# Kernel tuning notes

Hardware: AMD Instinct MI355X
Metric: run time of the kernel (lower is better)

The kernel has to match this reference:

```python
import jax, jax.numpy as jnp
import numpy as np
import math

D_MODEL = 2048
R = 512
N_HEADS = 16
D_K = R // N_HEADS  # 32
B = 2
S = 2048


def _xavier(key, out_dim, in_dim):
    limit = math.sqrt(6.0 / (in_dim + out_dim))
    return jax.random.uniform(key, (out_dim, in_dim), jnp.float32, -limit, limit)


def setup_inputs() -> dict:
    key = jax.random.key(0)
    ks = jax.random.split(key, 6)
    x = jax.random.normal(ks[0], (B, S, D_MODEL), dtype=jnp.float32)
    mask = jnp.ones((B, 1, 1, S), dtype=jnp.int32)
    # torch nn.Linear weights have shape (out, in)
    Wq = _xavier(ks[1], R, D_MODEL)
    Wk = _xavier(ks[2], R, D_MODEL)
    Wv = _xavier(ks[3], R, D_MODEL)
    Wo = _xavier(ks[4], D_MODEL, R)
    bq = jnp.zeros((R,), jnp.float32)
    bk = jnp.zeros((R,), jnp.float32)
    bv = jnp.zeros((R,), jnp.float32)
    bo = jnp.zeros((D_MODEL,), jnp.float32)
    return {"x": x, "Wq": Wq, "bq": bq, "Wk": Wk, "bk": bk,
            "Wv": Wv, "bv": bv, "Wo": Wo, "bo": bo, "mask": mask}


def reference(x, Wq, bq, Wk, bk, Wv, bv, Wo, bo, mask):
    b, s, _ = x.shape
    scale = math.sqrt(D_K)
    # projections: (B,S,d_model) @ (d_model,r) -> (B,S,r)
    Q = x @ Wq.T + bq
    K = x @ Wk.T + bk
    V = x @ Wv.T + bv
    # (B,S,r) -> (B,H,S,d_k)
    Q = Q.reshape(b, s, N_HEADS, D_K).transpose(0, 2, 1, 3)
    K = K.reshape(b, s, N_HEADS, D_K).transpose(0, 2, 1, 3)
    V = V.reshape(b, s, N_HEADS, D_K).transpose(0, 2, 1, 3)
    # scores: (B,H,Sq,Sk)
    scores = jnp.einsum('bhqd,bhkd->bhqk', Q, K) / scale
    scores = jnp.where(mask == 0, -jnp.inf, scores)
    attn = jax.nn.softmax(scores, axis=-1)  # dropout p=0 (eval)
    out = jnp.einsum('bhqk,bhkd->bhqd', attn, V)
    out = out.transpose(0, 2, 1, 3).reshape(b, s, R)
    return out @ Wo.T + bo
```

## Files before the change

### kernel.cpp

```cpp
#include <hip/hip_runtime.h>
#include <hip/hip_bf16.h>
#include <math.h>

typedef __attribute__((ext_vector_type(8))) short bf16x8;
typedef __attribute__((ext_vector_type(4))) float f32x4;

#define D_MODEL 2048
#define R_DIM 512
#define N_HEADS 16
#define D_K 32
#define B_SZ 2
#define SEQ 2048
#define M_ROWS (B_SZ * SEQ)
#define N_QKV 1536
#define QSCALE 0.2550627231338903f

__device__ __forceinline__ void dma16(const void* g, void* l)
{
    __builtin_amdgcn_global_load_lds(
        (const __attribute__((address_space(1))) void*)g,
        (__attribute__((address_space(3))) void*)l, 16, 0, 0);
}

__device__ __forceinline__ unsigned cvt_pk_bf16(float lo, float hi)
{
    unsigned r;
    asm("v_cvt_pk_bf16_f32 %0, %1, %2" : "=v"(r) : "v"(lo), "v"(hi));
    return r;
}

__global__ __launch_bounds__(256) void cvt_inputs(
    const float* __restrict__ x,  __hip_bfloat16* __restrict__ xb,
    const float* __restrict__ Wq, const float* __restrict__ Wk,
    const float* __restrict__ Wv, const float* __restrict__ Wo,
    __hip_bfloat16* __restrict__ Wqkvb, __hip_bfloat16* __restrict__ Wob,
    const float* __restrict__ bq, const float* __restrict__ bk,
    const float* __restrict__ bv, float* __restrict__ bias_qkv,
    const int* __restrict__ mask, float* __restrict__ mbias)
{
    const int by = blockIdx.y;
    const int tid = blockIdx.x * blockDim.x + threadIdx.x;
    const int nthr = gridDim.x * blockDim.x;
    if (by == 5) {
        for (int i = tid; i < N_QKV; i += nthr) {
            float v = (i < 512) ? bq[i] * QSCALE
                    : (i < 1024) ? bk[i - 512] : bv[i - 1024];
            bias_qkv[i] = v;
        }
        for (int i = tid; i < B_SZ * SEQ; i += nthr)
            mbias[i] = mask[i] ? 0.0f : -1e30f;
        return;
    }
    const float* src; __hip_bfloat16* dst; float sc = 1.0f; int n;
    switch (by) {
      case 0: src = Wq; dst = Wqkvb; sc = QSCALE; n = R_DIM * D_MODEL; break;
      case 1: src = Wk; dst = Wqkvb + (size_t)R_DIM * D_MODEL; n = R_DIM * D_MODEL; break;
      case 2: src = Wv; dst = Wqkvb + (size_t)2 * R_DIM * D_MODEL; n = R_DIM * D_MODEL; break;
      case 3: src = Wo; dst = Wob; n = D_MODEL * R_DIM; break;
      default: src = x;  dst = xb;  n = M_ROWS * D_MODEL; break;
    }
    const float4* s4 = (const float4*)src;
    ushort4* d4 = (ushort4*)dst;
    const int n4 = n >> 2;
    const int step = nthr * 4;
    for (int i0 = tid; i0 < n4; i0 += step) {
        float4 f0 = s4[i0];
        float4 f1 = s4[i0 + nthr];
        float4 f2 = s4[i0 + 2 * nthr];
        float4 f3 = s4[i0 + 3 * nthr];
        union { ushort4 u; __hip_bfloat16 h[4]; } r0, r1, r2, r3;
        r0.h[0] = __float2bfloat16(f0.x * sc); r0.h[1] = __float2bfloat16(f0.y * sc);
        r0.h[2] = __float2bfloat16(f0.z * sc); r0.h[3] = __float2bfloat16(f0.w * sc);
        r1.h[0] = __float2bfloat16(f1.x * sc); r1.h[1] = __float2bfloat16(f1.y * sc);
        r1.h[2] = __float2bfloat16(f1.z * sc); r1.h[3] = __float2bfloat16(f1.w * sc);
        r2.h[0] = __float2bfloat16(f2.x * sc); r2.h[1] = __float2bfloat16(f2.y * sc);
        r2.h[2] = __float2bfloat16(f2.z * sc); r2.h[3] = __float2bfloat16(f2.w * sc);
        r3.h[0] = __float2bfloat16(f3.x * sc); r3.h[1] = __float2bfloat16(f3.y * sc);
        r3.h[2] = __float2bfloat16(f3.z * sc); r3.h[3] = __float2bfloat16(f3.w * sc);
        d4[i0]            = r0.u;
        d4[i0 + nthr]     = r1.u;
        d4[i0 + 2 * nthr] = r2.u;
        d4[i0 + 3 * nthr] = r3.u;
    }
}

template<bool OUT_BF16>
__global__ __launch_bounds__(256, 3) void gemm_dma(
    const __hip_bfloat16* __restrict__ A,
    const __hip_bfloat16* __restrict__ W,
    const float* __restrict__ bias,
    void* __restrict__ Cv,
    int N, int K)
{
    __shared__ __hip_bfloat16 As[128 * 64];
    __shared__ __hip_bfloat16 Bs[128 * 64];

    const int tid = threadIdx.x, lane = tid & 63, w = tid >> 6;
    const int l15 = lane & 15, q = lane >> 4;
    const int bm = blockIdx.y * 128, bn = blockIdx.x * 128;
    const int m_off = (w & 1) * 64, n_off = (w >> 1) * 64;

    const int lrow = lane >> 3;
    const int lc   = (lane & 7) ^ lrow;

    f32x4 acc[4][4] = {};

    for (int kt = 0; kt < K; kt += 64) {
        if (kt) __syncthreads();
        #pragma unroll
        for (int j = 0; j < 4; j++) {
            int row = (w * 4 + j) * 8 + lrow;
            dma16(&A[(size_t)(bm + row) * K + kt + lc * 8], &As[(w * 4 + j) * 512]);
        }
        #pragma unroll
        for (int j = 0; j < 4; j++) {
            int row = (w * 4 + j) * 8 + lrow;
            dma16(&W[(size_t)(bn + row) * K + kt + lc * 8], &Bs[(w * 4 + j) * 512]);
        }
        __syncthreads();

        #pragma unroll
        for (int ks = 0; ks < 2; ks++) {
            bf16x8 af[4], bf[4];
            #pragma unroll
            for (int t = 0; t < 4; t++) {
                int row = m_off + t * 16 + l15;
                af[t] = *(const bf16x8*)&As[row * 64 + (((ks * 4 + q) ^ (l15 & 7)) * 8)];
            }
            #pragma unroll
            for (int u = 0; u < 4; u++) {
                int row = n_off + u * 16 + l15;
                bf[u] = *(const bf16x8*)&Bs[row * 64 + (((ks * 4 + q) ^ (l15 & 7)) * 8)];
            }
            #pragma unroll
            for (int mt = 0; mt < 4; mt++)
                #pragma unroll
                for (int nt = 0; nt < 4; nt++)
                    acc[mt][nt] = __builtin_amdgcn_mfma_f32_16x16x32_bf16(
                        af[mt], bf[nt], acc[mt][nt], 0, 0, 0);
        }
    }

    #pragma unroll
    for (int mt = 0; mt < 4; mt++) {
        #pragma unroll
        for (int nt = 0; nt < 4; nt++) {
            int gm = bm + m_off + mt * 16 + q * 4;
            int gn = bn + n_off + nt * 16 + l15;
            float bv = bias[gn];
            #pragma unroll
            for (int r = 0; r < 4; r++) {
                float v = acc[mt][nt][r] + bv;
                if (OUT_BF16)
                    ((__hip_bfloat16*)Cv)[(size_t)(gm + r) * N + gn] = __float2bfloat16(v);
                else
                    ((float*)Cv)[(size_t)(gm + r) * N + gn] = v;
            }
        }
    }
}

__global__ __launch_bounds__(256, 4) void flash_attn8(
    const __hip_bfloat16* __restrict__ QKV,
    const float* __restrict__ mbias,
    __hip_bfloat16* __restrict__ O)
{
    __shared__ __hip_bfloat16 Ks[2][64 * 40];
    __shared__ __hip_bfloat16 Vt[2][32 * 72];

    const int tid = threadIdx.x, lane = tid & 63, w = tid >> 6;
    const int l15 = lane & 15, qg = lane >> 4;

    const int nwg = (int)gridDim.x;
    const int swz = ((int)blockIdx.x & 7) * (nwg >> 3) + ((int)blockIdx.x >> 3);
    const int qt = swz & 15;
    const int h  = (swz >> 4) & 15;
    const int b  = swz >> 8;
    const int q0 = qt * 128;

    const bf16x8 qa0 = *(const bf16x8*)
        &QKV[(size_t)(b * SEQ + q0 + w * 32 + l15) * N_QKV + h * D_K + qg * 8];
    const bf16x8 qa1 = *(const bf16x8*)
        &QKV[(size_t)(b * SEQ + q0 + w * 32 + 16 + l15) * N_QKV + h * D_K + qg * 8];

    const int kv_k = tid >> 2, d0_k = (tid & 3) * 8;
    const int kv_v = tid & 63, d0_v = (tid >> 6) * 8;
    const int scol_v = (kv_v & 32) + ((kv_v >> 2) & 3) * 8
                     + ((kv_v >> 4) & 1) * 4 + (kv_v & 3);

    const __hip_bfloat16* Kp = QKV + (size_t)b * SEQ * N_QKV + R_DIM + h * D_K;
    const __hip_bfloat16* Vp = QKV + (size_t)b * SEQ * N_QKV + 2 * R_DIM + h * D_K;
    const float* mb_base = mbias + b * SEQ;

    f32x4 oaccA[2] = {};
    f32x4 oaccB[2] = {};
    float rsum0 = 0.f, rsum1 = 0.f;

    uint4 kregA, kregB, vregA, vregB;

    kregA = *(const uint4*)&Kp[(size_t)kv_k * N_QKV + d0_k];
    vregA = *(const uint4*)&Vp[(size_t)kv_v * N_QKV + d0_v];

#define FA_EXP(SC, MB, PA, U0, U1, RS)                                          \
    {                                                                           \
        float p0 = __builtin_amdgcn_exp2f(SC[0] + MB.x);                        \
        float p1 = __builtin_amdgcn_exp2f(SC[1] + MB.y);                        \
        float p2 = __builtin_amdgcn_exp2f(SC[2] + MB.z);                        \
        float p3 = __builtin_amdgcn_exp2f(SC[3] + MB.w);                        \
        RS += (p0 + p1) + (p2 + p3);                                            \
        PA.u[U0] = cvt_pk_bf16(p0, p1);                                         \
        PA.u[U1] = cvt_pk_bf16(p2, p3);                                         \
    }

#define FA_ITER(KT, BUF, KREG, VREG, KREGN, VREGN)                              \
    {                                                                           \
                  \
        *(uint4*)&Ks[BUF][kv_k * 40 + d0_k] = KREG;                             \
        { union { uint4 u; __hip_bfloat16 hv[8]; } vv; vv.u = VREG;             \
          _Pragma("unroll")                                                     \
          for (int j = 0; j < 8; j++)                                           \
              Vt[BUF][(d0_v + j) * 72 + scol_v] = vv.hv[j]; }                   \
        __syncthreads();                                                        \
         \
        float4 mb0 = *(const float4*)&mb_base[(KT) +  0 + qg * 4];              \
        float4 mb1 = *(const float4*)&mb_base[(KT) + 16 + qg * 4];              \
        float4 mb2 = *(const float4*)&mb_base[(KT) + 32 + qg * 4];              \
        float4 mb3 = *(const float4*)&mb_base[(KT) + 48 + qg * 4];              \
                 \
        if ((KT) + 64 < SEQ) {                                                  \
            KREGN = *(const uint4*)&Kp[(size_t)((KT) + 64 + kv_k) * N_QKV + d0_k]; \
            VREGN = *(const uint4*)&Vp[(size_t)((KT) + 64 + kv_v) * N_QKV + d0_v]; \
        }                                                                       \
                               \
        f32x4 a0, a1, a2, a3, b0, b1, b2, b3;                                   \
        __builtin_amdgcn_s_setprio(1);                                          \
        { bf16x8 kb = *(const bf16x8*)&Ks[BUF][( 0 + l15) * 40 + qg * 8];       \
          f32x4 z = {};                                                         \
          a0 = __builtin_amdgcn_mfma_f32_16x16x32_bf16(kb, qa0, z, 0, 0, 0);    \
          b0 = __builtin_amdgcn_mfma_f32_16x16x32_bf16(kb, qa1, z, 0, 0, 0); }  \
        { bf16x8 kb = *(const bf16x8*)&Ks[BUF][(16 + l15) * 40 + qg * 8];       \
          f32x4 z = {};                                                         \
          a1 = __builtin_amdgcn_mfma_f32_16x16x32_bf16(kb, qa0, z, 0, 0, 0);    \
          b1 = __builtin_amdgcn_mfma_f32_16x16x32_bf16(kb, qa1, z, 0, 0, 0); }  \
        { bf16x8 kb = *(const bf16x8*)&Ks[BUF][(32 + l15) * 40 + qg * 8];       \
          f32x4 z = {};                                                         \
          a2 = __builtin_amdgcn_mfma_f32_16x16x32_bf16(kb, qa0, z, 0, 0, 0);    \
          b2 = __builtin_amdgcn_mfma_f32_16x16x32_bf16(kb, qa1, z, 0, 0, 0); }  \
        { bf16x8 kb = *(const bf16x8*)&Ks[BUF][(48 + l15) * 40 + qg * 8];       \
          f32x4 z = {};                                                         \
          a3 = __builtin_amdgcn_mfma_f32_16x16x32_bf16(kb, qa0, z, 0, 0, 0);    \
          b3 = __builtin_amdgcn_mfma_f32_16x16x32_bf16(kb, qa1, z, 0, 0, 0); }  \
        __builtin_amdgcn_s_setprio(0);                                          \
              \
        union { unsigned u[4]; bf16x8 v; } paA0, paA1, paB0, paB1;              \
        FA_EXP(a0, mb0, paA0, 0, 1, rsum0)                                      \
        FA_EXP(a1, mb1, paA0, 2, 3, rsum0)                                      \
        FA_EXP(a2, mb2, paA1, 0, 1, rsum0)                                      \
        FA_EXP(a3, mb3, paA1, 2, 3, rsum0)                                      \
        FA_EXP(b0, mb0, paB0, 0, 1, rsum1)                                      \
        FA_EXP(b1, mb1, paB0, 2, 3, rsum1)                                      \
        FA_EXP(b2, mb2, paB1, 0, 1, rsum1)                                      \
        FA_EXP(b3, mb3, paB1, 2, 3, rsum1)                                      \
                      \
        __builtin_amdgcn_s_setprio(1);                                          \
        _Pragma("unroll")                                                       \
        for (int dt = 0; dt < 2; dt++) {                                        \
            const __hip_bfloat16* vrow = &Vt[BUF][(dt * 16 + l15) * 72];        \
            bf16x8 vb0 = *(const bf16x8*)&vrow[qg * 8];                         \
            bf16x8 vb1 = *(const bf16x8*)&vrow[32 + qg * 8];                    \
            oaccA[dt] = __builtin_amdgcn_mfma_f32_16x16x32_bf16(paA0.v, vb0, oaccA[dt], 0, 0, 0); \
            oaccA[dt] = __builtin_amdgcn_mfma_f32_16x16x32_bf16(paA1.v, vb1, oaccA[dt], 0, 0, 0); \
            oaccB[dt] = __builtin_amdgcn_mfma_f32_16x16x32_bf16(paB0.v, vb0, oaccB[dt], 0, 0, 0); \
            oaccB[dt] = __builtin_amdgcn_mfma_f32_16x16x32_bf16(paB1.v, vb1, oaccB[dt], 0, 0, 0); \
        }                                                                       \
        __builtin_amdgcn_s_setprio(0);                                          \
    }

    for (int kt = 0; kt < SEQ; kt += 128) {
        FA_ITER(kt,      0, kregA, vregA, kregB, vregB)
        FA_ITER(kt + 64, 1, kregB, vregB, kregA, vregA)
    }
#undef FA_ITER
#undef FA_EXP

    float s0 = rsum0, s1 = rsum1;
    s0 += __shfl_xor(s0, 16, 64);
    s0 += __shfl_xor(s0, 32, 64);
    s1 += __shfl_xor(s1, 16, 64);
    s1 += __shfl_xor(s1, 32, 64);

    #pragma unroll
    for (int r = 0; r < 4; r++) {
        float invA = 1.0f / __shfl(s0, qg * 4 + r, 64);
        float invB = 1.0f / __shfl(s1, qg * 4 + r, 64);
        int rowA = q0 + w * 32 + qg * 4 + r;
        int rowB = rowA + 16;
        #pragma unroll
        for (int dt = 0; dt < 2; dt++) {
            O[(size_t)(b * SEQ + rowA) * R_DIM + h * D_K + dt * 16 + l15] =
                __float2bfloat16(oaccA[dt][r] * invA);
            O[(size_t)(b * SEQ + rowB) * R_DIM + h * D_K + dt * 16 + l15] =
                __float2bfloat16(oaccB[dt][r] * invB);
        }
    }
}

extern "C" void kernel_launch(void* const* d_in, const int* in_sizes, int n_in,
                              void* d_out, int out_size, void* d_ws, size_t ws_size,
                              hipStream_t stream)
{
    const float* x  = (const float*)d_in[0];
    const float* Wq = (const float*)d_in[1];
    const float* bq = (const float*)d_in[2];
    const float* Wk = (const float*)d_in[3];
    const float* bk = (const float*)d_in[4];
    const float* Wv = (const float*)d_in[5];
    const float* bv = (const float*)d_in[6];
    const float* Wo = (const float*)d_in[7];
    const float* bo = (const float*)d_in[8];
    const int* mask = (const int*)d_in[9];
    float* out = (float*)d_out;

    char* p = (char*)d_ws;
    __hip_bfloat16* xb     = (__hip_bfloat16*)p;
    __hip_bfloat16* AO     = xb;
    __hip_bfloat16* Wqkvb  = (__hip_bfloat16*)(p + (16u << 20));
    __hip_bfloat16* Wob    = (__hip_bfloat16*)(p + (22u << 20));
    float*          biasq  = (float*)(p + (24u << 20));
    float*          mbias  = (float*)(p + (24u << 20) + 8192);
    __hip_bfloat16* QKVb   = (__hip_bfloat16*)(p + (25u << 20));

    dim3 blk(256);
    hipLaunchKernelGGL(cvt_inputs, dim3(256, 6), blk, 0, stream,
                       x, xb, Wq, Wk, Wv, Wo, Wqkvb, Wob, bq, bk, bv, biasq, mask, mbias);
    hipLaunchKernelGGL((gemm_dma<true>), dim3(N_QKV / 128, M_ROWS / 128), blk, 0, stream,
                       xb, Wqkvb, biasq, QKVb, N_QKV, D_MODEL);
    hipLaunchKernelGGL(flash_attn8, dim3(B_SZ * N_HEADS * (SEQ / 128)), blk, 0, stream,
                       QKVb, mbias, AO);
    hipLaunchKernelGGL((gemm_dma<false>), dim3(D_MODEL / 128, M_ROWS / 128), blk, 0, stream,
                       AO, Wob, bo, out, D_MODEL, R_DIM);
}
```

Before: 193.2 us.

## Double-buffer GEMM LDS tiles, raise MFMA priority, narrow output GEMM tile

The GEMM kernel now double-buffers its A and B LDS tiles. The next K-tile's DMA is issued before computing on the current one, so global loads overlap MFMA work. MFMA blocks are wrapped in s_setprio to favour compute issue. The output projection GEMM uses a 64-wide N tile, which doubles its grid to fill more CUs, at the cost of doubled LDS (64KB for BN=128) that may reduce occupancy below the launch-bounds target.

```diff
diff --git a/kernel.cpp b/kernel.cpp
--- a/kernel.cpp
+++ b/kernel.cpp
@@ -84,7 +84,7 @@
     }
 }
 
-template<bool OUT_BF16>
+template<bool OUT_BF16, int BN>
 __global__ __launch_bounds__(256, 3) void gemm_dma(
     const __hip_bfloat16* __restrict__ A,
     const __hip_bfloat16* __restrict__ W,
@@ -92,59 +92,71 @@
     void* __restrict__ Cv,
     int N, int K)
 {
-    __shared__ __hip_bfloat16 As[128 * 64];
-    __shared__ __hip_bfloat16 Bs[128 * 64];
+    constexpr int NF = BN / 32;
+    __shared__ __hip_bfloat16 As[2][128 * 64];
+    __shared__ __hip_bfloat16 Bs[2][BN * 64];
 
     const int tid = threadIdx.x, lane = tid & 63, w = tid >> 6;
     const int l15 = lane & 15, q = lane >> 4;
-    const int bm = blockIdx.y * 128, bn = blockIdx.x * 128;
-    const int m_off = (w & 1) * 64, n_off = (w >> 1) * 64;
+    const int bm = blockIdx.y * 128, bn = blockIdx.x * BN;
+    const int m_off = (w & 1) * 64, n_off = (w >> 1) * (BN / 2);
 
     const int lrow = lane >> 3;
     const int lc   = (lane & 7) ^ lrow;
 
-    f32x4 acc[4][4] = {};
-
-    for (int kt = 0; kt < K; kt += 64) {
-        if (kt) __syncthreads();
-        #pragma unroll
-        for (int j = 0; j < 4; j++) {
-            int row = (w * 4 + j) * 8 + lrow;
-            dma16(&A[(size_t)(bm + row) * K + kt + lc * 8], &As[(w * 4 + j) * 512]);
-        }
-        #pragma unroll
-        for (int j = 0; j < 4; j++) {
-            int row = (w * 4 + j) * 8 + lrow;
-            dma16(&W[(size_t)(bn + row) * K + kt + lc * 8], &Bs[(w * 4 + j) * 512]);
-        }
+    f32x4 acc[4][NF] = {};
+
+#define G_STAGE(BUF, KT)                                                        \
+    {                                                                           \
+        _Pragma("unroll")                                                       \
+        for (int j = 0; j < 4; j++) {                          \
+            int row = (w * 4 + j) * 8 + lrow;                                   \
+            dma16(&A[(size_t)(bm + row) * K + (KT) + lc * 8],                   \
+                  &As[BUF][(w * 4 + j) * 512]);                                 \
+        }                                                                       \
+        _Pragma("unroll")                                                       \
+        for (int j = 0; j < NF; j++) {                          \
+            int row = (w * NF + j) * 8 + lrow;                                  \
+            dma16(&W[(size_t)(bn + row) * K + (KT) + lc * 8],                   \
+                  &Bs[BUF][(w * NF + j) * 512]);                                \
+        }                                                                       \
+    }
+
+    G_STAGE(0, 0)
+    int t = 0;
+    for (int kt = 0; kt < K; kt += 64, t ^= 1) {
         __syncthreads();
+        if (kt + 64 < K) G_STAGE(t ^ 1, kt + 64)
 
         #pragma unroll
         for (int ks = 0; ks < 2; ks++) {
-            bf16x8 af[4], bf[4];
+            bf16x8 af[4], bf[NF];
             #pragma unroll
-            for (int t = 0; t < 4; t++) {
-                int row = m_off + t * 16 + l15;
-                af[t] = *(const bf16x8*)&As[row * 64 + (((ks * 4 + q) ^ (l15 & 7)) * 8)];
+            for (int mt = 0; mt < 4; mt++) {
+                int row = m_off + mt * 16 + l15;
+                af[mt] = *(const bf16x8*)&As[t][row * 64 + (((ks * 4 + q) ^ (l15 & 7)) * 8)];
             }
             #pragma unroll
-            for (int u = 0; u < 4; u++) {
+            for (int u = 0; u < NF; u++) {
                 int row = n_off + u * 16 + l15;
-                bf[u] = *(const bf16x8*)&Bs[row * 64 + (((ks * 4 + q) ^ (l15 & 7)) * 8)];
+                bf[u] = *(const bf16x8*)&Bs[t][row * 64 + (((ks * 4 + q) ^ (l15 & 7)) * 8)];
             }
+            __builtin_amdgcn_s_setprio(1);
             #pragma unroll
             for (int mt = 0; mt < 4; mt++)
                 #pragma unroll
-                for (int nt = 0; nt < 4; nt++)
+                for (int nt = 0; nt < NF; nt++)
                     acc[mt][nt] = __builtin_amdgcn_mfma_f32_16x16x32_bf16(
                         af[mt], bf[nt], acc[mt][nt], 0, 0, 0);
+            __builtin_amdgcn_s_setprio(0);
         }
     }
+#undef G_STAGE
 
     #pragma unroll
     for (int mt = 0; mt < 4; mt++) {
         #pragma unroll
-        for (int nt = 0; nt < 4; nt++) {
+        for (int nt = 0; nt < NF; nt++) {
             int gm = bm + m_off + mt * 16 + q * 4;
             int gn = bn + n_off + nt * 16 + l15;
             float bv = bias[gn];
@@ -333,10 +345,10 @@
     dim3 blk(256);
     hipLaunchKernelGGL(cvt_inputs, dim3(256, 6), blk, 0, stream,
                        x, xb, Wq, Wk, Wv, Wo, Wqkvb, Wob, bq, bk, bv, biasq, mask, mbias);
-    hipLaunchKernelGGL((gemm_dma<true>), dim3(N_QKV / 128, M_ROWS / 128), blk, 0, stream,
+    hipLaunchKernelGGL((gemm_dma<true, 128>), dim3(N_QKV / 128, M_ROWS / 128), blk, 0, stream,
                        xb, Wqkvb, biasq, QKVb, N_QKV, D_MODEL);
     hipLaunchKernelGGL(flash_attn8, dim3(B_SZ * N_HEADS * (SEQ / 128)), blk, 0, stream,
                        QKVb, mbias, AO);
-    hipLaunchKernelGGL((gemm_dma<false>), dim3(D_MODEL / 128, M_ROWS / 128), blk, 0, stream,
+    hipLaunchKernelGGL((gemm_dma<false, 64>), dim3(D_MODEL / 64, M_ROWS / 128), blk, 0, stream,
                        AO, Wob, bo, out, D_MODEL, R_DIM);
 }
```

Result: no change. 194.6 us (+0.7%).
